# Kernel optimization log

Hardware: AMD Instinct MI355X
Metric: run time of the kernel (lower is better)

Reference implementation:

```python
import jax, jax.numpy as jnp
import numpy as np

N_NODES = 100000
N_EDGES = 800000
D_DATA = 100
H_DIM = 256
N_CLS = 47
K = 10
ALPHA = 0.1


def setup_inputs() -> dict:
    key = jax.random.key(0)
    ks = jax.random.split(key, 7)
    x = jax.random.normal(ks[0], (N_NODES, D_DATA), dtype=jnp.float32)
    src = jax.random.randint(ks[1], (N_EDGES,), 0, N_NODES, dtype=jnp.int32)
    dst = jax.random.randint(ks[2], (N_EDGES,), 0, N_NODES, dtype=jnp.int32)
    W1 = jax.random.normal(ks[3], (D_DATA, H_DIM), dtype=jnp.float32) / np.sqrt(D_DATA)
    b1 = jax.random.normal(ks[4], (H_DIM,), dtype=jnp.float32) * 0.01
    W2 = jax.random.normal(ks[5], (H_DIM, N_CLS), dtype=jnp.float32) / np.sqrt(H_DIM)
    b2 = jax.random.normal(ks[6], (N_CLS,), dtype=jnp.float32) * 0.01
    return {"x": x, "src": src, "dst": dst, "W1": W1, "b1": b1, "W2": W2, "b2": b2}


def reference(x, src, dst, W1, b1, W2, b2):
    # --- APPNPConv: K steps of symmetric-normalized SpMM + teleport ---
    # DGL normalizes with in-degree^{-1/2} on both message source and output.
    deg = jax.ops.segment_sum(jnp.ones((N_EDGES,), x.dtype), dst, num_segments=N_NODES)
    norm = jax.lax.rsqrt(jnp.maximum(deg, 1.0))[:, None]  # [N,1]
    h = x
    for _ in range(K):
        msg = (h * norm)[src]                              # gather src feats, [E,D]
        agg = jax.ops.segment_sum(msg, dst, num_segments=N_NODES)
        h = (1.0 - ALPHA) * (agg * norm) + ALPHA * x
    # --- feat_trans MLP (dropout inactive in eval) ---
    z = jax.nn.relu(h @ W1 + b1)
    logits = z @ W2 + b2
    return logits
```

## Files before the change

### kernel.cpp

```cpp
#include <hip/hip_runtime.h>
#include <hip/hip_fp16.h>


#define N_NODES 100000
#define N_PAD   100032
#define N_EDGES 800000
#define D_DATA  100
#define H_DIM   256
#define N_CLS   47
#define K_STEPS 10
#define ALPHA   0.1f
#define HS      128
#define MB      64

#define SCAN_NB    200
#define SCAN_CHUNK 500
#define EW_CAP (N_EDGES + 3 * N_NODES)

typedef _Float16 half8_t __attribute__((ext_vector_type(8)));
typedef float floatx4 __attribute__((ext_vector_type(4)));


__global__ void deg_kernel(const int* __restrict__ dst, int* __restrict__ deg,
                           int* __restrict__ slot, int e) {
    int i = blockIdx.x * blockDim.x + threadIdx.x;
    if (i < e) slot[i] = atomicAdd(&deg[dst[i]], 1);
}

__global__ __launch_bounds__(256) void scan_partial_kernel(
        const int* __restrict__ deg, int* __restrict__ partials) {
    __shared__ int red[256];
    int t = threadIdx.x;
    int base = blockIdx.x * SCAN_CHUNK;
    int s = 0;
    int i0 = 2 * t, i1 = 2 * t + 1;
    if (i0 < SCAN_CHUNK) s += (deg[base + i0] + 3) & ~3;
    if (i1 < SCAN_CHUNK) s += (deg[base + i1] + 3) & ~3;
    red[t] = s;
    __syncthreads();
    for (int off = 128; off > 0; off >>= 1) {
        if (t < off) red[t] += red[t + off];
        __syncthreads();
    }
    if (t == 0) partials[blockIdx.x] = red[0];
}

__global__ __launch_bounds__(256) void scan_top_kernel(
        const int* __restrict__ partials, int* __restrict__ pofs,
        int* __restrict__ row_ptr) {
    __shared__ int s[256];
    int t = threadIdx.x;
    s[t] = (t < SCAN_NB) ? partials[t] : 0;
    __syncthreads();
    for (int off = 1; off < 256; off <<= 1) {
        int v = (t >= off) ? s[t - off] : 0;
        __syncthreads();
        s[t] += v;
        __syncthreads();
    }
    if (t < SCAN_NB) pofs[t] = s[t] - partials[t];
    if (t == SCAN_NB - 1) row_ptr[N_NODES] = s[t];
}

__global__ __launch_bounds__(256) void scan_emit_kernel(
        const int* __restrict__ deg, const int* __restrict__ pofs,
        int* __restrict__ row_ptr, float* __restrict__ norm) {
    __shared__ int s[256];
    int t = threadIdx.x;
    int base = blockIdx.x * SCAN_CHUNK;
    int i0 = 2 * t, i1 = 2 * t + 1;
    int d0 = (i0 < SCAN_CHUNK) ? deg[base + i0] : 0;
    int d1 = (i1 < SCAN_CHUNK) ? deg[base + i1] : 0;
    int p0 = (d0 + 3) & ~3, p1 = (d1 + 3) & ~3;
    s[t] = p0 + p1;
    __syncthreads();
    for (int off = 1; off < 256; off <<= 1) {
        int v = (t >= off) ? s[t - off] : 0;
        __syncthreads();
        s[t] += v;
        __syncthreads();
    }
    int p = s[t] - (p0 + p1) + pofs[blockIdx.x];
    if (i0 < SCAN_CHUNK) {
        row_ptr[base + i0] = p;
        norm[base + i0] = rsqrtf((float)max(d0, 1));
    }
    if (i1 < SCAN_CHUNK) {
        row_ptr[base + i1] = p + p0;
        norm[base + i1] = rsqrtf((float)max(d1, 1));
    }
}

__global__ void scatter_kernel(const int* __restrict__ src, const int* __restrict__ dst,
                               const int* __restrict__ slot,
                               const int* __restrict__ row_ptr,
                               int* __restrict__ es, int e) {
    int i = blockIdx.x * blockDim.x + threadIdx.x;
    if (i < e) es[row_ptr[dst[i]] + slot[i]] = src[i];
}

__global__ void pad_kernel(const int* __restrict__ deg, const int* __restrict__ row_ptr,
                           int* __restrict__ es, int n) {
    int i = blockIdx.x * blockDim.x + threadIdx.x;
    if (i < n) {
        int b = row_ptr[i] + deg[i];
        int e = row_ptr[i + 1];
        for (int s = b; s < e; ++s) es[s] = N_NODES;
    }
}

__global__ void pack_w1_kernel(const float* __restrict__ W1, __half* __restrict__ W1p) {
    int idx = blockIdx.x * blockDim.x + threadIdx.x;
    if (idx >= 16 * 4 * 64 * 8) return;
    int j = idx & 7;
    int lane = (idx >> 3) & 63;
    int ks = (idx >> 9) & 3;
    int nt = idx >> 11;
    int k = ks * 32 + (lane >> 4) * 8 + j;
    int n = nt * 16 + (lane & 15);
    float v = (k < D_DATA) ? W1[(size_t)k * H_DIM + n] : 0.f;
    W1p[idx] = __float2half(v);
}

__global__ void pack_w2_kernel(const float* __restrict__ W2, __half* __restrict__ W2p) {
    int idx = blockIdx.x * blockDim.x + threadIdx.x;
    if (idx >= 3 * 8 * 64 * 8) return;
    int j = idx & 7;
    int lane = (idx >> 3) & 63;
    int ks = (idx >> 9) & 7;
    int nt = idx >> 12;
    int k = ks * 32 + (lane >> 4) * 8 + j;
    int n = nt * 16 + (lane & 15);
    float v = (n < N_CLS) ? W2[(size_t)k * N_CLS + n] : 0.f;
    W2p[idx] = __float2half(v);
}

__global__ void convert_xhat_kernel(const float* __restrict__ x,
                                    const float* __restrict__ norm,
                                    __half2* __restrict__ xh, int n_half2) {
    int i = blockIdx.x * blockDim.x + threadIdx.x;
    if (i < n_half2) {
        int node = i >> 6;
        int c2 = i & 63;
        float2 v = make_float2(0.f, 0.f);
        if (node < N_NODES && c2 < D_DATA / 2) {
            float nn = norm[node];
            const float2* r = (const float2*)(x + (size_t)node * D_DATA);
            float2 xv = r[c2];
            v = make_float2(nn * xv.x, nn * xv.y);
        }
        xh[i] = __float22half2_rn(v);
    }
}

__global__ void zero_rows_kernel(__half2* __restrict__ a, __half2* __restrict__ b) {
    int i = threadIdx.x;
    if (i < 64) a[(size_t)N_NODES * (HS / 2) + i] = __half2();
    else        b[(size_t)N_NODES * (HS / 2) + (i - 64)] = __half2();
}


__global__ __launch_bounds__(256) void prop_mid_kernel(
        const __half* __restrict__ hin, const __half* __restrict__ xhat,
        const float* __restrict__ norm, const int* __restrict__ row_ptr,
        const int* __restrict__ es, __half* __restrict__ hout, int n_nodes) {
    int lane = threadIdx.x & 63;
    int wave = blockIdx.x * 4 + (threadIdx.x >> 6);
    int nA = __builtin_amdgcn_readfirstlane(wave * 2);
    if (nA >= n_nodes) return;
    int nB = nA + 1;
    int begA = __builtin_amdgcn_readfirstlane(row_ptr[nA]);
    int begB = __builtin_amdgcn_readfirstlane(row_ptr[nB]);
    int endB = __builtin_amdgcn_readfirstlane(row_ptr[nB + 1]);
    int nbA = (begB - begA) >> 2;
    int nbB = (endB - begB) >> 2;
    int mb = nbA > nbB ? nbA : nbB;

    float a0x = 0.f, a0y = 0.f, a1x = 0.f, a1y = 0.f;
    float b0x = 0.f, b0y = 0.f, b1x = 0.f, b1y = 0.f;
    for (int it = 0; it < mb; ++it) {
        bool doA = it < nbA, doB = it < nbB;
        int sA[4], sB[4];
        if (doA) {
            int e = begA + it * 4;
#pragma unroll
            for (int j = 0; j < 4; ++j) sA[j] = es[e + j];
        }
        if (doB) {
            int e = begB + it * 4;
#pragma unroll
            for (int j = 0; j < 4; ++j) sB[j] = es[e + j];
        }
        __half2 hvA[4], hvB[4];
        if (doA) {
#pragma unroll
            for (int j = 0; j < 4; ++j)
                hvA[j] = ((const __half2*)(hin + (size_t)sA[j] * HS))[lane];
        }
        if (doB) {
#pragma unroll
            for (int j = 0; j < 4; ++j)
                hvB[j] = ((const __half2*)(hin + (size_t)sB[j] * HS))[lane];
        }
        if (doA) {
            float2 v0 = __half22float2(hvA[0]), v1 = __half22float2(hvA[1]);
            float2 v2 = __half22float2(hvA[2]), v3 = __half22float2(hvA[3]);
            a0x += v0.x + v2.x; a0y += v0.y + v2.y;
            a1x += v1.x + v3.x; a1y += v1.y + v3.y;
        }
        if (doB) {
            float2 v0 = __half22float2(hvB[0]), v1 = __half22float2(hvB[1]);
            float2 v2 = __half22float2(hvB[2]), v3 = __half22float2(hvB[3]);
            b0x += v0.x + v2.x; b0y += v0.y + v2.y;
            b1x += v1.x + v3.x; b1y += v1.y + v3.y;
        }
    }
    {
        float nn = norm[nA];
        float c = (1.0f - ALPHA) * nn * nn;
        float2 t = __half22float2(((const __half2*)(xhat + (size_t)nA * HS))[lane]);
        float2 o = make_float2(c * (a0x + a1x) + ALPHA * t.x,
                               c * (a0y + a1y) + ALPHA * t.y);
        ((__half2*)(hout + (size_t)nA * HS))[lane] = __float22half2_rn(o);
    }
    {
        float nn = norm[nB];
        float c = (1.0f - ALPHA) * nn * nn;
        float2 t = __half22float2(((const __half2*)(xhat + (size_t)nB * HS))[lane]);
        float2 o = make_float2(c * (b0x + b1x) + ALPHA * t.x,
                               c * (b0y + b1y) + ALPHA * t.y);
        ((__half2*)(hout + (size_t)nB * HS))[lane] = __float22half2_rn(o);
    }
}

__global__ __launch_bounds__(256) void prop_final_kernel(
        const __half* __restrict__ hin, const float* __restrict__ x,
        const float* __restrict__ norm, const int* __restrict__ row_ptr,
        const int* __restrict__ es, __half* __restrict__ hout, int n_nodes) {
    int lane = threadIdx.x & 63;
    int wave = blockIdx.x * 4 + (threadIdx.x >> 6);
    int nA = __builtin_amdgcn_readfirstlane(wave * 2);
    if (nA >= n_nodes) return;
    int nB = nA + 1;
    int begA = __builtin_amdgcn_readfirstlane(row_ptr[nA]);
    int begB = __builtin_amdgcn_readfirstlane(row_ptr[nB]);
    int endB = __builtin_amdgcn_readfirstlane(row_ptr[nB + 1]);
    int nbA = (begB - begA) >> 2;
    int nbB = (endB - begB) >> 2;
    int mb = nbA > nbB ? nbA : nbB;

    float a0x = 0.f, a0y = 0.f, a1x = 0.f, a1y = 0.f;
    float b0x = 0.f, b0y = 0.f, b1x = 0.f, b1y = 0.f;
    for (int it = 0; it < mb; ++it) {
        bool doA = it < nbA, doB = it < nbB;
        int sA[4], sB[4];
        if (doA) {
            int e = begA + it * 4;
#pragma unroll
            for (int j = 0; j < 4; ++j) sA[j] = es[e + j];
        }
        if (doB) {
            int e = begB + it * 4;
#pragma unroll
            for (int j = 0; j < 4; ++j) sB[j] = es[e + j];
        }
        __half2 hvA[4], hvB[4];
        if (doA) {
#pragma unroll
            for (int j = 0; j < 4; ++j)
                hvA[j] = ((const __half2*)(hin + (size_t)sA[j] * HS))[lane];
        }
        if (doB) {
#pragma unroll
            for (int j = 0; j < 4; ++j)
                hvB[j] = ((const __half2*)(hin + (size_t)sB[j] * HS))[lane];
        }
        if (doA) {
            float2 v0 = __half22float2(hvA[0]), v1 = __half22float2(hvA[1]);
            float2 v2 = __half22float2(hvA[2]), v3 = __half22float2(hvA[3]);
            a0x += v0.x + v2.x; a0y += v0.y + v2.y;
            a1x += v1.x + v3.x; a1y += v1.y + v3.y;
        }
        if (doB) {
            float2 v0 = __half22float2(hvB[0]), v1 = __half22float2(hvB[1]);
            float2 v2 = __half22float2(hvB[2]), v3 = __half22float2(hvB[3]);
            b0x += v0.x + v2.x; b0y += v0.y + v2.y;
            b1x += v1.x + v3.x; b1y += v1.y + v3.y;
        }
    }
    {
        float c = (1.0f - ALPHA) * norm[nA];
        float2 xv = make_float2(0.f, 0.f);
        if (lane < D_DATA / 2)
            xv = ((const float2*)(x + (size_t)nA * D_DATA))[lane];
        float2 o = make_float2(c * (a0x + a1x) + ALPHA * xv.x,
                               c * (a0y + a1y) + ALPHA * xv.y);
        ((__half2*)(hout + (size_t)nA * HS))[lane] = __float22half2_rn(o);
    }
    {
        float c = (1.0f - ALPHA) * norm[nB];
        float2 xv = make_float2(0.f, 0.f);
        if (lane < D_DATA / 2)
            xv = ((const float2*)(x + (size_t)nB * D_DATA))[lane];
        float2 o = make_float2(c * (b0x + b1x) + ALPHA * xv.x,
                               c * (b0y + b1y) + ALPHA * xv.y);
        ((__half2*)(hout + (size_t)nB * HS))[lane] = __float22half2_rn(o);
    }
}


#define ZP 264

__global__ __launch_bounds__(256, 4) void mlp_mfma_kernel(
        const __half* __restrict__ h16,
        const __half* __restrict__ W1p, const float* __restrict__ b1,
        const __half* __restrict__ W2p, const float* __restrict__ b2,
        float* __restrict__ out, int n_nodes) {
    __shared__ _Float16 zs[MB][ZP];
    int tid = threadIdx.x;
    int lane = tid & 63;
    int w = tid >> 6;
    int q = lane >> 4;
    int r = lane & 15;
    int node0 = blockIdx.x * MB + w * 16;

    half8_t a1[4];
#pragma unroll
    for (int ks = 0; ks < 4; ++ks)
        a1[ks] = *(const half8_t*)(h16 + (size_t)(node0 + r) * HS + ks * 32 + q * 8);

    const half8_t* w1f = (const half8_t*)W1p;
#pragma unroll 4
    for (int nt = 0; nt < 16; ++nt) {
        floatx4 acc = {0.f, 0.f, 0.f, 0.f};
#pragma unroll
        for (int ks = 0; ks < 4; ++ks) {
            half8_t b = w1f[(nt * 4 + ks) * 64 + lane];
            acc = __builtin_amdgcn_mfma_f32_16x16x32_f16(a1[ks], b, acc, 0, 0, 0);
        }
        float bb = b1[nt * 16 + r];
#pragma unroll
        for (int reg = 0; reg < 4; ++reg) {
            float zv = fmaxf(acc[reg] + bb, 0.f);
            zs[w * 16 + q * 4 + reg][nt * 16 + r] = (_Float16)zv;
        }
    }

    half8_t a2[8];
#pragma unroll
    for (int ks = 0; ks < 8; ++ks)
        a2[ks] = *(const half8_t*)&zs[w * 16 + r][ks * 32 + q * 8];

    const half8_t* w2f = (const half8_t*)W2p;
#pragma unroll
    for (int nt = 0; nt < 3; ++nt) {
        floatx4 acc = {0.f, 0.f, 0.f, 0.f};
#pragma unroll
        for (int ks = 0; ks < 8; ++ks) {
            half8_t b = w2f[(nt * 8 + ks) * 64 + lane];
            acc = __builtin_amdgcn_mfma_f32_16x16x32_f16(a2[ks], b, acc, 0, 0, 0);
        }
        int c = nt * 16 + r;
        if (c < N_CLS) {
            float bb = b2[c];
#pragma unroll
            for (int reg = 0; reg < 4; ++reg) {
                int node = node0 + q * 4 + reg;
                if (node < n_nodes)
                    out[(size_t)node * N_CLS + c] = acc[reg] + bb;
            }
        }
    }
}


static inline size_t align_up(size_t v, size_t a) { return (v + a - 1) & ~(a - 1); }

extern "C" void kernel_launch(void* const* d_in, const int* in_sizes, int n_in,
                              void* d_out, int out_size, void* d_ws, size_t ws_size,
                              hipStream_t stream) {
    const float* x   = (const float*)d_in[0];
    const int*   src = (const int*)d_in[1];
    const int*   dst = (const int*)d_in[2];
    const float* W1  = (const float*)d_in[3];
    const float* b1  = (const float*)d_in[4];
    const float* W2  = (const float*)d_in[5];
    const float* b2  = (const float*)d_in[6];
    float* out = (float*)d_out;

    char* p = (char*)d_ws;
    size_t off = 0;
    int* deg = (int*)(p + off);           off = align_up(off + N_NODES * 4, 256);
    int* row_ptr = (int*)(p + off);       off = align_up(off + (N_NODES + 1) * 4, 256);
    int* slot = (int*)(p + off);          off = align_up(off + (size_t)N_EDGES * 4, 256);
    float* norm = (float*)(p + off);      off = align_up(off + N_NODES * 4, 256);
    int* partials = (int*)(p + off);      off = align_up(off + SCAN_NB * 4, 256);
    int* pofs = (int*)(p + off);          off = align_up(off + SCAN_NB * 4, 256);
    __half* W1p = (__half*)(p + off);     off = align_up(off + 16 * 4 * 64 * 8 * 2, 256);
    __half* W2p = (__half*)(p + off);     off = align_up(off + 3 * 8 * 64 * 8 * 2, 256);
    int* es = (int*)(p + off);            off = align_up(off + (size_t)EW_CAP * 4, 256);
    __half* xhat = (__half*)(p + off);    off = align_up(off + (size_t)N_PAD * HS * 2, 256);
    __half* h16A = (__half*)(p + off);    off = align_up(off + (size_t)N_PAD * HS * 2, 256);
    __half* h16B = (__half*)(p + off);    off = align_up(off + (size_t)N_PAD * HS * 2, 256);
    (void)ws_size;

    hipMemsetAsync(deg, 0, N_NODES * 4, stream);

    int eb = (N_EDGES + 255) / 256;
    deg_kernel<<<eb, 256, 0, stream>>>(dst, deg, slot, N_EDGES);
    scan_partial_kernel<<<SCAN_NB, 256, 0, stream>>>(deg, partials);
    scan_top_kernel<<<1, 256, 0, stream>>>(partials, pofs, row_ptr);
    scan_emit_kernel<<<SCAN_NB, 256, 0, stream>>>(deg, pofs, row_ptr, norm);
    scatter_kernel<<<eb, 256, 0, stream>>>(src, dst, slot, row_ptr, es, N_EDGES);
    pad_kernel<<<(N_NODES + 255) / 256, 256, 0, stream>>>(deg, row_ptr, es, N_NODES);
    pack_w1_kernel<<<128, 256, 0, stream>>>(W1, W1p);
    pack_w2_kernel<<<48, 256, 0, stream>>>(W2, W2p);

    int nh2 = (N_NODES + 1) * (HS / 2);
    convert_xhat_kernel<<<(nh2 + 255) / 256, 256, 0, stream>>>(x, norm, (__half2*)xhat, nh2);
    zero_rows_kernel<<<1, 128, 0, stream>>>((__half2*)h16A, (__half2*)h16B);

    int pb = (N_NODES / 2) / 4;
    prop_mid_kernel<<<pb, 256, 0, stream>>>(xhat, xhat, norm, row_ptr, es, h16A, N_NODES);
    const __half* hin = h16A;
    for (int k = 1; k < K_STEPS - 1; ++k) {
        __half* ho = (k & 1) ? h16B : h16A;
        prop_mid_kernel<<<pb, 256, 0, stream>>>(hin, xhat, norm, row_ptr, es, ho, N_NODES);
        hin = ho;
    }
    prop_final_kernel<<<pb, 256, 0, stream>>>(hin, x, norm, row_ptr, es, h16B, N_NODES);

    int mb = (N_NODES + MB - 1) / MB;
    mlp_mfma_kernel<<<mb, 256, 0, stream>>>(h16B, W1p, b1, W2p, b2, out, N_NODES);
}
```

Before: 553.2 us.

## Restructure SpMM to 4 nodes per wave with 16-byte gathers and index prefetch

The propagation kernel now gives each wave four destination nodes. Each 16-lane group loads one neighbour's full 128-half row as 16-byte vectors, where the old code had each lane load a half2 from every neighbour. The next iteration's edge indices are prefetched before the current gathers are accumulated, and partial sums are combined across groups with shuffles. The mid and final kernels are merged into one template. The aim is fewer, wider memory transactions and more gathers in flight, at the cost of more registers and extra cross-lane reductions.

```diff
diff --git a/kernel.cpp b/kernel.cpp
--- a/kernel.cpp
+++ b/kernel.cpp
@@ -16,6 +16,7 @@
 #define SCAN_NB    200
 #define SCAN_CHUNK 500
 #define EW_CAP (N_EDGES + 3 * N_NODES)
+#define EW_LAST (EW_CAP - 1)
 
 typedef _Float16 half8_t __attribute__((ext_vector_type(8)));
 typedef float floatx4 __attribute__((ext_vector_type(4)));
@@ -160,152 +161,113 @@
 }
 
 
-__global__ __launch_bounds__(256) void prop_mid_kernel(
+template <bool FINAL>
+__global__ __launch_bounds__(256) void prop_kernel(
         const __half* __restrict__ hin, const __half* __restrict__ xhat,
+        const float* __restrict__ xf,
         const float* __restrict__ norm, const int* __restrict__ row_ptr,
         const int* __restrict__ es, __half* __restrict__ hout, int n_nodes) {
     int lane = threadIdx.x & 63;
     int wave = blockIdx.x * 4 + (threadIdx.x >> 6);
-    int nA = __builtin_amdgcn_readfirstlane(wave * 2);
-    if (nA >= n_nodes) return;
-    int nB = nA + 1;
-    int begA = __builtin_amdgcn_readfirstlane(row_ptr[nA]);
-    int begB = __builtin_amdgcn_readfirstlane(row_ptr[nB]);
-    int endB = __builtin_amdgcn_readfirstlane(row_ptr[nB + 1]);
-    int nbA = (begB - begA) >> 2;
-    int nbB = (endB - begB) >> 2;
-    int mb = nbA > nbB ? nbA : nbB;
-
-    float a0x = 0.f, a0y = 0.f, a1x = 0.f, a1y = 0.f;
-    float b0x = 0.f, b0y = 0.f, b1x = 0.f, b1y = 0.f;
+    int n0 = __builtin_amdgcn_readfirstlane(wave * 4);
+    if (n0 >= n_nodes) return;
+    int g = lane >> 4;
+    int c = lane & 15;
+
+    int rp[5];
+#pragma unroll
+    for (int j = 0; j < 5; ++j)
+        rp[j] = __builtin_amdgcn_readfirstlane(row_ptr[n0 + j]);
+    int beg[4], nb[4];
+#pragma unroll
+    for (int j = 0; j < 4; ++j) {
+        beg[j] = rp[j];
+        nb[j] = (rp[j + 1] - rp[j]) >> 2;
+    }
+    int mb = max(max(nb[0], nb[1]), max(nb[2], nb[3]));
+
+    float accf[4][8];
+#pragma unroll
+    for (int j = 0; j < 4; ++j)
+#pragma unroll
+        for (int k = 0; k < 8; ++k) accf[j][k] = 0.f;
+
+    int idxc[4];
+#pragma unroll
+    for (int j = 0; j < 4; ++j) {
+        int e = beg[j] + g;
+        if (e > EW_LAST) e = EW_LAST;
+        int v = es[e];
+        idxc[j] = (0 < nb[j]) ? v : N_NODES;
+    }
+
     for (int it = 0; it < mb; ++it) {
-        bool doA = it < nbA, doB = it < nbB;
-        int sA[4], sB[4];
-        if (doA) {
-            int e = begA + it * 4;
-#pragma unroll
-            for (int j = 0; j < 4; ++j) sA[j] = es[e + j];
-        }
-        if (doB) {
-            int e = begB + it * 4;
-#pragma unroll
-            for (int j = 0; j < 4; ++j) sB[j] = es[e + j];
-        }
-        __half2 hvA[4], hvB[4];
-        if (doA) {
-#pragma unroll
-            for (int j = 0; j < 4; ++j)
-                hvA[j] = ((const __half2*)(hin + (size_t)sA[j] * HS))[lane];
-        }
-        if (doB) {
-#pragma unroll
-            for (int j = 0; j < 4; ++j)
-                hvB[j] = ((const __half2*)(hin + (size_t)sB[j] * HS))[lane];
-        }
-        if (doA) {
-            float2 v0 = __half22float2(hvA[0]), v1 = __half22float2(hvA[1]);
-            float2 v2 = __half22float2(hvA[2]), v3 = __half22float2(hvA[3]);
-            a0x += v0.x + v2.x; a0y += v0.y + v2.y;
-            a1x += v1.x + v3.x; a1y += v1.y + v3.y;
-        }
-        if (doB) {
-            float2 v0 = __half22float2(hvB[0]), v1 = __half22float2(hvB[1]);
-            float2 v2 = __half22float2(hvB[2]), v3 = __half22float2(hvB[3]);
-            b0x += v0.x + v2.x; b0y += v0.y + v2.y;
-            b1x += v1.x + v3.x; b1y += v1.y + v3.y;
-        }
-    }
-    {
-        float nn = norm[nA];
-        float c = (1.0f - ALPHA) * nn * nn;
-        float2 t = __half22float2(((const __half2*)(xhat + (size_t)nA * HS))[lane]);
-        float2 o = make_float2(c * (a0x + a1x) + ALPHA * t.x,
-                               c * (a0y + a1y) + ALPHA * t.y);
-        ((__half2*)(hout + (size_t)nA * HS))[lane] = __float22half2_rn(o);
-    }
-    {
-        float nn = norm[nB];
-        float c = (1.0f - ALPHA) * nn * nn;
-        float2 t = __half22float2(((const __half2*)(xhat + (size_t)nB * HS))[lane]);
-        float2 o = make_float2(c * (b0x + b1x) + ALPHA * t.x,
-                               c * (b0y + b1y) + ALPHA * t.y);
-        ((__half2*)(hout + (size_t)nB * HS))[lane] = __float22half2_rn(o);
-    }
-}
-
-__global__ __launch_bounds__(256) void prop_final_kernel(
-        const __half* __restrict__ hin, const float* __restrict__ x,
-        const float* __restrict__ norm, const int* __restrict__ row_ptr,
-        const int* __restrict__ es, __half* __restrict__ hout, int n_nodes) {
-    int lane = threadIdx.x & 63;
-    int wave = blockIdx.x * 4 + (threadIdx.x >> 6);
-    int nA = __builtin_amdgcn_readfirstlane(wave * 2);
-    if (nA >= n_nodes) return;
-    int nB = nA + 1;
-    int begA = __builtin_amdgcn_readfirstlane(row_ptr[nA]);
-    int begB = __builtin_amdgcn_readfirstlane(row_ptr[nB]);
-    int endB = __builtin_amdgcn_readfirstlane(row_ptr[nB + 1]);
-    int nbA = (begB - begA) >> 2;
-    int nbB = (endB - begB) >> 2;
-    int mb = nbA > nbB ? nbA : nbB;
-
-    float a0x = 0.f, a0y = 0.f, a1x = 0.f, a1y = 0.f;
-    float b0x = 0.f, b0y = 0.f, b1x = 0.f, b1y = 0.f;
-    for (int it = 0; it < mb; ++it) {
-        bool doA = it < nbA, doB = it < nbB;
-        int sA[4], sB[4];
-        if (doA) {
-            int e = begA + it * 4;
-#pragma unroll
-            for (int j = 0; j < 4; ++j) sA[j] = es[e + j];
-        }
-        if (doB) {
-            int e = begB + it * 4;
-#pragma unroll
-            for (int j = 0; j < 4; ++j) sB[j] = es[e + j];
-        }
-        __half2 hvA[4], hvB[4];
-        if (doA) {
-#pragma unroll
-            for (int j = 0; j < 4; ++j)
-                hvA[j] = ((const __half2*)(hin + (size_t)sA[j] * HS))[lane];
-        }
-        if (doB) {
-#pragma unroll
-            for (int j = 0; j < 4; ++j)
-                hvB[j] = ((const __half2*)(hin + (size_t)sB[j] * HS))[lane];
-        }
-        if (doA) {
-            float2 v0 = __half22float2(hvA[0]), v1 = __half22float2(hvA[1]);
-            float2 v2 = __half22float2(hvA[2]), v3 = __half22float2(hvA[3]);
-            a0x += v0.x + v2.x; a0y += v0.y + v2.y;
-            a1x += v1.x + v3.x; a1y += v1.y + v3.y;
-        }
-        if (doB) {
-            float2 v0 = __half22float2(hvB[0]), v1 = __half22float2(hvB[1]);
-            float2 v2 = __half22float2(hvB[2]), v3 = __half22float2(hvB[3]);
-            b0x += v0.x + v2.x; b0y += v0.y + v2.y;
-            b1x += v1.x + v3.x; b1y += v1.y + v3.y;
-        }
-    }
-    {
-        float c = (1.0f - ALPHA) * norm[nA];
-        float2 xv = make_float2(0.f, 0.f);
-        if (lane < D_DATA / 2)
-            xv = ((const float2*)(x + (size_t)nA * D_DATA))[lane];
-        float2 o = make_float2(c * (a0x + a1x) + ALPHA * xv.x,
-                               c * (a0y + a1y) + ALPHA * xv.y);
-        ((__half2*)(hout + (size_t)nA * HS))[lane] = __float22half2_rn(o);
-    }
-    {
-        float c = (1.0f - ALPHA) * norm[nB];
-        float2 xv = make_float2(0.f, 0.f);
-        if (lane < D_DATA / 2)
-            xv = ((const float2*)(x + (size_t)nB * D_DATA))[lane];
-        float2 o = make_float2(c * (b0x + b1x) + ALPHA * xv.x,
-                               c * (b0y + b1y) + ALPHA * xv.y);
-        ((__half2*)(hout + (size_t)nB * HS))[lane] = __float22half2_rn(o);
-    }
+        half8_t hv0 = *(const half8_t*)(hin + (size_t)idxc[0] * HS + (c << 3));
+        half8_t hv1 = *(const half8_t*)(hin + (size_t)idxc[1] * HS + (c << 3));
+        half8_t hv2 = *(const half8_t*)(hin + (size_t)idxc[2] * HS + (c << 3));
+        half8_t hv3 = *(const half8_t*)(hin + (size_t)idxc[3] * HS + (c << 3));
+
+        int idxn[4];
+        int itn = it + 1;
+#pragma unroll
+        for (int j = 0; j < 4; ++j) {
+            int e = beg[j] + itn * 4 + g;
+            if (e > EW_LAST) e = EW_LAST;
+            int v = es[e];
+            idxn[j] = (itn < nb[j]) ? v : N_NODES;
+        }
+
+#pragma unroll
+        for (int k = 0; k < 8; ++k) accf[0][k] += (float)hv0[k];
+#pragma unroll
+        for (int k = 0; k < 8; ++k) accf[1][k] += (float)hv1[k];
+#pragma unroll
+        for (int k = 0; k < 8; ++k) accf[2][k] += (float)hv2[k];
+#pragma unroll
+        for (int k = 0; k < 8; ++k) accf[3][k] += (float)hv3[k];
+
+#pragma unroll
+        for (int j = 0; j < 4; ++j) idxc[j] = idxn[j];
+    }
+
+#pragma unroll
+    for (int j = 0; j < 4; ++j)
+#pragma unroll
+        for (int k = 0; k < 8; ++k) {
+            float v = accf[j][k];
+            v += __shfl_xor(v, 16, 64);
+            v += __shfl_xor(v, 32, 64);
+            accf[j][k] = v;
+        }
+
+    float tot[8];
+#pragma unroll
+    for (int k = 0; k < 8; ++k)
+        tot[k] = g == 0 ? accf[0][k]
+               : g == 1 ? accf[1][k]
+               : g == 2 ? accf[2][k] : accf[3][k];
+
+    int n = n0 + g;
+    half8_t o;
+    if (!FINAL) {
+        float nn = norm[n];
+        float cf = (1.0f - ALPHA) * nn * nn;
+        half8_t xv = *(const half8_t*)(xhat + (size_t)n * HS + (c << 3));
+#pragma unroll
+        for (int k = 0; k < 8; ++k)
+            o[k] = (_Float16)(cf * tot[k] + ALPHA * (float)xv[k]);
+    } else {
+        float cf = (1.0f - ALPHA) * norm[n];
+        const float* xr = xf + (size_t)n * D_DATA + c * 8;
+        float xv[8];
+#pragma unroll
+        for (int k = 0; k < 8; ++k)
+            xv[k] = (c * 8 + k < D_DATA) ? xr[k] : 0.f;
+#pragma unroll
+        for (int k = 0; k < 8; ++k)
+            o[k] = (_Float16)(cf * tot[k] + ALPHA * xv[k]);
+    }
+    *(half8_t*)(hout + (size_t)n * HS + (c << 3)) = o;
 }
 
 
@@ -360,14 +322,14 @@
             half8_t b = w2f[(nt * 8 + ks) * 64 + lane];
             acc = __builtin_amdgcn_mfma_f32_16x16x32_f16(a2[ks], b, acc, 0, 0, 0);
         }
-        int c = nt * 16 + r;
-        if (c < N_CLS) {
-            float bb = b2[c];
+        int cix = nt * 16 + r;
+        if (cix < N_CLS) {
+            float bb = b2[cix];
 #pragma unroll
             for (int reg = 0; reg < 4; ++reg) {
                 int node = node0 + q * 4 + reg;
                 if (node < n_nodes)
-                    out[(size_t)node * N_CLS + c] = acc[reg] + bb;
+                    out[(size_t)node * N_CLS + cix] = acc[reg] + bb;
             }
         }
     }
@@ -420,16 +382,16 @@
     convert_xhat_kernel<<<(nh2 + 255) / 256, 256, 0, stream>>>(x, norm, (__half2*)xhat, nh2);
     zero_rows_kernel<<<1, 128, 0, stream>>>((__half2*)h16A, (__half2*)h16B);
 
-    int pb = (N_NODES / 2) / 4;
-    prop_mid_kernel<<<pb, 256, 0, stream>>>(xhat, xhat, norm, row_ptr, es, h16A, N_NODES);
+    int pb = N_NODES / 16;
+    prop_kernel<false><<<pb, 256, 0, stream>>>(xhat, xhat, nullptr, norm, row_ptr, es, h16A, N_NODES);
     const __half* hin = h16A;
     for (int k = 1; k < K_STEPS - 1; ++k) {
         __half* ho = (k & 1) ? h16B : h16A;
-        prop_mid_kernel<<<pb, 256, 0, stream>>>(hin, xhat, norm, row_ptr, es, ho, N_NODES);
+        prop_kernel<false><<<pb, 256, 0, stream>>>(hin, xhat, nullptr, norm, row_ptr, es, ho, N_NODES);
         hin = ho;
     }
-    prop_final_kernel<<<pb, 256, 0, stream>>>(hin, x, norm, row_ptr, es, h16B, N_NODES);
-
-    int mb = (N_NODES + MB - 1) / MB;
-    mlp_mfma_kernel<<<mb, 256, 0, stream>>>(h16B, W1p, b1, W2p, b2, out, N_NODES);
-}
+    prop_kernel<true><<<pb, 256, 0, stream>>>(hin, nullptr, x, norm, row_ptr, es, h16B, N_NODES);
+
+    int mbk = (N_NODES + MB - 1) / MB;
+    mlp_mfma_kernel<<<mbk, 256, 0, stream>>>(h16B, W1p, b1, W2p, b2, out, N_NODES);
+}
```

Measured after the change: 618.8 us. 11.9% more time.
